# Optimization experiments

Measured on AMD Instinct MI355X. Metric: run time of the kernel, lower is better.

## Reference

```python
import jax, jax.numpy as jnp
import numpy as np

PROJ_DIM = 16384  # self.projDim / output_dim
THRESH = 1e-8     # self.thresh


def setup_inputs() -> dict:
    key = jax.random.key(0)
    k1, k2, k3, k4, k5 = jax.random.split(key, 5)
    B, C, H, W = 16, 2048, 14, 14
    x = jax.random.normal(k1, (B, C, H, W), dtype=jnp.float32)
    # count-sketch hash indices and Rademacher signs (fixed random params of CBP)
    h1 = jax.random.randint(k2, (C,), 0, PROJ_DIM, dtype=jnp.int32)
    h2 = jax.random.randint(k3, (C,), 0, PROJ_DIM, dtype=jnp.int32)
    w1 = (2 * jax.random.randint(k4, (C,), 0, 2) - 1).astype(jnp.float32)
    w2 = (2 * jax.random.randint(k5, (C,), 0, 2) - 1).astype(jnp.float32)
    return {"x": x, "w1": w1, "w2": w2, "h1": h1, "h2": h2}


def _count_sketch(xf, w, h):
    # xf: (N, C); scatter-add signed features into PROJ_DIM bins per location
    N = xf.shape[0]
    return jnp.zeros((N, PROJ_DIM), xf.dtype).at[:, h].add(xf * w)


def reference(x, w1, w2, h1, h2):
    B, C, H, W = x.shape
    # (B, C, H, W) -> (B*H*W, C): one feature vector per spatial location
    xf = x.transpose(0, 2, 3, 1).reshape(B * H * W, C)
    s1 = _count_sketch(xf, w1, h1)  # (N, D)
    s2 = _count_sketch(xf, w2, h2)  # (N, D)
    # circular convolution of the two sketches via FFT (real input -> rfft)
    y = jnp.fft.irfft(jnp.fft.rfft(s1, axis=-1) * jnp.fft.rfft(s2, axis=-1),
                      n=PROJ_DIM, axis=-1)  # (N, D)
    # sum-pool over spatial locations
    y = y.reshape(B, H * W, PROJ_DIM).sum(axis=1)  # (B, D)
    # signed sqrt + L2 normalization
    y = jnp.sign(y) * jnp.sqrt(jnp.abs(y) + THRESH)
    y = y / jnp.sqrt(jnp.sum(y * y, axis=-1, keepdims=True) + THRESH)
    return y  # (B, 16384), already flat as in torch.flatten(..., 1)
```

## Files before the change

### kernel.cpp

```cpp
#include <hip/hip_runtime.h>


#define D_PROJ 16384
#define C_CH   2048
#define HW_N   196
#define NKS    7
#define KPAD   (NKS * 32)
#define B_N    16
#define THREADS 512
#define NT     64
#define BUFS   6
#define ROWSH  448
#define TILE_SH (16 * ROWSH)
#define FPSCALE 65536.0f
#define INVSCALE (1.0f / 65536.0f)

typedef short  short8 __attribute__((ext_vector_type(8)));
typedef float  f32x4  __attribute__((ext_vector_type(4)));
typedef int    i32x4  __attribute__((ext_vector_type(4)));

static __device__ inline unsigned short f2bf(float f) {
    union { float f; unsigned u; } a; a.f = f;
    unsigned u = a.u;
    return (unsigned short)((u + 0x7FFFu + ((u >> 16) & 1u)) >> 16);
}
static __device__ inline float bf2f(unsigned short h) {
    union { unsigned u; float f; } a; a.u = ((unsigned)h) << 16;
    return a.f;
}
static __device__ inline f32x4 mfma16(short8 a, short8 b, f32x4 c) {
    return __builtin_amdgcn_mfma_f32_16x16x32_bf16(a, b, c, 0, 0, 0);
}

static __device__ inline void lds_iadd(int* p, int v) {
    unsigned off = (unsigned)(uintptr_t)p;
    asm volatile("ds_add_u32 %0, %1" :: "v"(off), "v"(v) : "memory");
}
static __device__ inline void lds_fadd(float* p, float v) {
    unsigned off = (unsigned)(uintptr_t)p;
    asm volatile("ds_add_f32 %0, %1" :: "v"(off), "v"(v) : "memory");
}
static __device__ inline void lds_drain() {
    asm volatile("s_waitcnt lgkmcnt(0)" ::: "memory");
    __builtin_amdgcn_sched_barrier(0);
}

static __device__ inline int swz_off(int ks, int lo64, int sub16, int row7) {
    return (((ks << 7) | lo64 | (sub16 << 4)) ^ (row7 << 4));
}

__global__ __launch_bounds__(256)
void cbp_convert(const float* __restrict__ x, unsigned short* __restrict__ ws) {
    const int id = blockIdx.x * 256 + threadIdx.x;
    const int total = B_N * C_CH * (KPAD / 8);
    if (id >= total) return;
    const int row = id / (KPAD / 8);
    const int sub = id - row * (KPAD / 8);
    const int k0  = sub * 8;
    const int ks  = k0 >> 5;
    const int s16 = (k0 >> 3) & 3;

    const float* xr = x + (size_t)row * HW_N;
    float v[8];
    if (k0 + 8 <= HW_N) {
        f32x4 p0 = *(const f32x4*)(xr + k0);
        f32x4 p1 = *(const f32x4*)(xr + k0 + 4);
#pragma unroll
        for (int e = 0; e < 4; ++e) { v[e] = p0[e]; v[4 + e] = p1[e]; }
    } else {
#pragma unroll
        for (int e = 0; e < 8; ++e) {
            const int k = k0 + e;
            v[e] = (k < HW_N) ? xr[k] : 0.0f;
        }
    }
    short8 hv, lv;
#pragma unroll
    for (int e = 0; e < 8; ++e) {
        unsigned short h = f2bf(v[e]);
        hv[e] = (short)h;
        lv[e] = (short)f2bf(v[e] - bf2f(h));
    }
    char* rowB = (char*)ws + (size_t)row * (ROWSH * 2);
    const int r7 = row & 7;
    *(short8*)(rowB + swz_off(ks, 0,  s16, r7)) = hv;
    *(short8*)(rowB + swz_off(ks, 64, s16, r7)) = lv;
}

static __device__ inline void stage_issue(const unsigned short* __restrict__ src0,
                                          unsigned short* dst0, int wave, int lane) {
    if (lane < 56) {
#pragma unroll
        for (int hlf = 0; hlf < 2; ++hlf) {
            const int row = wave + hlf * 8;
            const unsigned short* s = src0 + (size_t)row * ROWSH + (size_t)lane * 8;
            unsigned short* d = dst0 + (size_t)row * ROWSH;
            __builtin_amdgcn_global_load_lds(
                (const __attribute__((address_space(1))) void*)s,
                (__attribute__((address_space(3))) void*)d, 16, 0, 0);
        }
    }
}

__global__ __launch_bounds__(THREADS, 2)
void cbp_gram12(const unsigned short* __restrict__ ws,
                const float* __restrict__ w1f,
                const float* __restrict__ w2f,
                const int*   __restrict__ h1,
                const int*   __restrict__ h2,
                int*         __restrict__ part) {
    __shared__ __align__(16) int hist[D_PROJ];
    __shared__ __align__(16) unsigned short stage[BUFS][TILE_SH];
    __shared__ int pairsh[1024];

    const int id   = blockIdx.x;
    const int b    = ((id & 7) << 1) | ((id >> 3) & 1);
    const int rest = id >> 4;
    const int j0   = (rest & 1) * 1024;
    const int i0   = (rest >> 1) * 256;

    const int tid  = threadIdx.x;
    const int wave = tid >> 6;
    const int lane = tid & 63;
    const int l15  = lane & 15;
    const int lgrp = lane >> 4;
    const int r7s  = (l15 & 7) << 4;

    for (int t = tid; t < D_PROJ / 4; t += THREADS)
        ((i32x4*)hist)[t] = i32x4{0, 0, 0, 0};
    for (int t = tid; t < 1024; t += THREADS)
        pairsh[t] = h2[j0 + t] | (w2f[j0 + t] < 0.f ? (int)0x80000000 : 0);

    short8 ah[2][NKS], al[2][NKS];
    int    binr[2][4];
    float  s1s[2][4];
#pragma unroll
    for (int s = 0; s < 2; ++s) {
        const int irow = i0 + wave * 32 + s * 16 + l15;
        const char* rowA = (const char*)(ws + ((size_t)b * C_CH + irow) * ROWSH);
#pragma unroll
        for (int ks = 0; ks < NKS; ++ks) {
            ah[s][ks] = *(const short8*)(rowA + (((ks << 7) | (lgrp << 4)) ^ r7s));
            al[s][ks] = *(const short8*)(rowA + (((ks << 7) | 64 | (lgrp << 4)) ^ r7s));
        }
#pragma unroll
        for (int r = 0; r < 4; ++r) {
            const int ir = i0 + wave * 32 + s * 16 + lgrp * 4 + r;
            binr[s][r] = h1[ir];
            s1s[s][r]  = w1f[ir] * FPSCALE;
        }
    }

    const unsigned short* jbase = ws + ((size_t)b * C_CH + j0) * ROWSH;
#pragma unroll
    for (int p = 0; p < 4; ++p)
        stage_issue(jbase + (size_t)p * TILE_SH, stage[p], wave, lane);
    asm volatile("s_waitcnt lgkmcnt(0)" ::: "memory");

    for (int t = 0; t < NT; t += 2) {
        asm volatile("s_waitcnt vmcnt(4)" ::: "memory");
        __builtin_amdgcn_sched_barrier(0);
        asm volatile("s_barrier" ::: "memory");
        __builtin_amdgcn_sched_barrier(0);

        const int rb = t % BUFS;
#pragma unroll
        for (int half = 0; half < 2; ++half) {
            const int tt  = t + half;
            const char* srow = (const char*)&stage[rb + half][(size_t)l15 * ROWSH];
            f32x4 a0 = {0.f,0.f,0.f,0.f}, a1 = {0.f,0.f,0.f,0.f};
            f32x4 b0 = {0.f,0.f,0.f,0.f}, b1 = {0.f,0.f,0.f,0.f};
#pragma unroll
            for (int ks = 0; ks < NKS; ++ks) {
                const short8 bh = *(const short8*)(srow + (((ks << 7) | (lgrp << 4)) ^ r7s));
                const short8 bl = *(const short8*)(srow + (((ks << 7) | 64 | (lgrp << 4)) ^ r7s));
                if (ks & 1) {
                    a1 = mfma16(ah[0][ks], bh, a1);  b1 = mfma16(ah[1][ks], bh, b1);
                    a1 = mfma16(al[0][ks], bh, a1);  b1 = mfma16(al[1][ks], bh, b1);
                    a1 = mfma16(ah[0][ks], bl, a1);  b1 = mfma16(ah[1][ks], bl, b1);
                } else {
                    a0 = mfma16(ah[0][ks], bh, a0);  b0 = mfma16(ah[1][ks], bh, b0);
                    a0 = mfma16(al[0][ks], bh, a0);  b0 = mfma16(al[1][ks], bh, b0);
                    a0 = mfma16(ah[0][ks], bl, a0);  b0 = mfma16(ah[1][ks], bl, b0);
                }
            }
            const unsigned pk  = (unsigned)pairsh[tt * 16 + l15];
            const int      h2v = (int)(pk & 0x3FFFu);
            const unsigned sg2 = pk & 0x80000000u;
            const f32x4 g0 = a0 + a1;
            const f32x4 g1 = b0 + b1;
#pragma unroll
            for (int r = 0; r < 4; ++r) {
                int bin = binr[0][r] + h2v;
                if (bin >= D_PROJ) bin -= D_PROJ;
                const float fv = __uint_as_float(__float_as_uint(g0[r] * s1s[0][r]) ^ sg2);
                lds_iadd(&hist[bin], (int)rintf(fv));
            }
#pragma unroll
            for (int r = 0; r < 4; ++r) {
                int bin = binr[1][r] + h2v;
                if (bin >= D_PROJ) bin -= D_PROJ;
                const float fv = __uint_as_float(__float_as_uint(g1[r] * s1s[1][r]) ^ sg2);
                lds_iadd(&hist[bin], (int)rintf(fv));
            }
        }

        int t4 = t + 4; if (t4 > NT - 1) t4 = NT - 1;
        int t5 = t + 5; if (t5 > NT - 1) t5 = NT - 1;
        const int sb = (t + 4) % BUFS;
        stage_issue(jbase + (size_t)t4 * TILE_SH, stage[sb],     wave, lane);
        stage_issue(jbase + (size_t)t5 * TILE_SH, stage[sb + 1], wave, lane);
    }

    lds_drain();
    __syncthreads();
    int* pslot = part + (size_t)(b * 16 + rest) * D_PROJ;
    for (int t = tid; t < D_PROJ / 4; t += THREADS)
        ((i32x4*)pslot)[t] = ((const i32x4*)hist)[t];
}

__global__ void cbp_finalize2(const int* __restrict__ part, float* __restrict__ y) {
    const int b   = blockIdx.x;
    const int tid = threadIdx.x;
    const int* pb = part + (size_t)b * 16 * D_PROJ;
    float* yb = y + (size_t)b * D_PROJ;
    __shared__ float partial[4];

    float ssum = 0.f;
    for (int t = tid; t < D_PROJ; t += 256) {
        int acc = 0;
#pragma unroll
        for (int s = 0; s < 16; ++s) acc += pb[(size_t)s * D_PROJ + t];
        float v = (float)acc * INVSCALE;
        float sg = copysignf(sqrtf(fabsf(v) + 1e-8f), v);
        yb[t] = sg;
        ssum += sg * sg;
    }
    const int lane = tid & 63, wv = tid >> 6;
#pragma unroll
    for (int off = 32; off > 0; off >>= 1) ssum += __shfl_down(ssum, off, 64);
    if (lane == 0) partial[wv] = ssum;
    __syncthreads();
    const float total = partial[0] + partial[1] + partial[2] + partial[3];
    const float inv = 1.0f / sqrtf(total + 1e-8f);
    for (int t = tid; t < D_PROJ; t += 256) yb[t] *= inv;
}

static __device__ inline void cvt_split(const float (&v)[8], short8& hi, short8& lo) {
#pragma unroll
    for (int e = 0; e < 8; ++e) {
        unsigned short h = f2bf(v[e]);
        hi[e] = (short)h;
        lo[e] = (short)f2bf(v[e] - bf2f(h));
    }
}

__global__ __launch_bounds__(256, 2)
void cbp_gram_scatter(const float* __restrict__ x,
                      const float* __restrict__ w1f,
                      const float* __restrict__ w2f,
                      const int*   __restrict__ h1,
                      const int*   __restrict__ h2,
                      float*       __restrict__ y) {
    __shared__ float hist[D_PROJ];
    const int b    = blockIdx.y;
    const int i0   = blockIdx.x * 64;
    const int tid  = threadIdx.x;
    const int wave = tid >> 6;
    const int lane = tid & 63;
    const int l15  = lane & 15;
    const int lgrp = lane >> 4;

    for (int t = tid; t < D_PROJ; t += 256) hist[t] = 0.0f;
    const float* xb = x + (size_t)b * (C_CH * HW_N);

    const int    irow = i0 + wave * 16 + l15;
    const float* xa   = xb + (size_t)irow * HW_N;
    const float  w1s  = w1f[irow];
    short8 a_hi[NKS], a_lo[NKS];
#pragma unroll
    for (int ks = 0; ks < NKS; ++ks) {
        const int k0 = ks * 32 + lgrp * 8;
        float v[8];
#pragma unroll
        for (int e = 0; e < 8; ++e) {
            const int k = k0 + e;
            v[e] = (k < HW_N) ? xa[k] * w1s : 0.0f;
        }
        cvt_split(v, a_hi[ks], a_lo[ks]);
    }
    int bin1[4];
#pragma unroll
    for (int r = 0; r < 4; ++r) bin1[r] = h1[i0 + wave * 16 + lgrp * 4 + r];

    __syncthreads();

    for (int jt = 0; jt < C_CH / 16; ++jt) {
        const int    jrow = jt * 16 + l15;
        const float* xj   = xb + (size_t)jrow * HW_N;
        const float  w2s  = w2f[jrow];
        const int    h2j  = h2[jrow];
        f32x4 acc0 = {0.f, 0.f, 0.f, 0.f};
        f32x4 acc1 = {0.f, 0.f, 0.f, 0.f};
#pragma unroll
        for (int ks = 0; ks < NKS; ++ks) {
            const int k0 = ks * 32 + lgrp * 8;
            float v[8];
            if (ks < 6) {
                f32x4 p0 = *(const f32x4*)(xj + k0);
                f32x4 p1 = *(const f32x4*)(xj + k0 + 4);
#pragma unroll
                for (int e = 0; e < 4; ++e) { v[e] = p0[e]; v[4 + e] = p1[e]; }
            } else {
#pragma unroll
                for (int e = 0; e < 8; ++e) {
                    const int k = k0 + e;
                    v[e] = (k < HW_N) ? xj[k] : 0.0f;
                }
            }
#pragma unroll
            for (int e = 0; e < 8; ++e) v[e] *= w2s;
            short8 bhi, blo;
            cvt_split(v, bhi, blo);
            if (ks & 1) {
                acc1 = mfma16(a_hi[ks], bhi, acc1);
                acc1 = mfma16(a_hi[ks], blo, acc1);
                acc1 = mfma16(a_lo[ks], bhi, acc1);
            } else {
                acc0 = mfma16(a_hi[ks], bhi, acc0);
                acc0 = mfma16(a_hi[ks], blo, acc0);
                acc0 = mfma16(a_lo[ks], bhi, acc0);
            }
        }
        const f32x4 g = acc0 + acc1;
#pragma unroll
        for (int r = 0; r < 4; ++r) {
            int bin = bin1[r] + h2j;
            if (bin >= D_PROJ) bin -= D_PROJ;
            lds_fadd(&hist[bin], g[r]);
        }
    }

    lds_drain();
    __syncthreads();
    float* yb = y + (size_t)b * D_PROJ;
    for (int t = tid; t < D_PROJ; t += 256)
        atomicAdd(&yb[t], hist[t]);
}

__global__ void cbp_finalize(float* __restrict__ y) {
    const int b   = blockIdx.x;
    const int tid = threadIdx.x;
    float* yb = y + (size_t)b * D_PROJ;
    __shared__ float partial[4];

    float ssum = 0.f;
    for (int t = tid; t < D_PROJ; t += 256) {
        float v = yb[t];
        float s = copysignf(sqrtf(fabsf(v) + 1e-8f), v);
        yb[t] = s;
        ssum += s * s;
    }
    const int lane = tid & 63, wv = tid >> 6;
#pragma unroll
    for (int off = 32; off > 0; off >>= 1) ssum += __shfl_down(ssum, off, 64);
    if (lane == 0) partial[wv] = ssum;
    __syncthreads();
    const float total = partial[0] + partial[1] + partial[2] + partial[3];
    const float inv = 1.0f / sqrtf(total + 1e-8f);
    for (int t = tid; t < D_PROJ; t += 256) yb[t] *= inv;
}

extern "C" void kernel_launch(void* const* d_in, const int* in_sizes, int n_in,
                              void* d_out, int out_size, void* d_ws, size_t ws_size,
                              hipStream_t stream) {
    const float* x  = (const float*)d_in[0];
    const float* w1 = (const float*)d_in[1];
    const float* w2 = (const float*)d_in[2];
    const int*   h1 = (const int*)d_in[3];
    const int*   h2 = (const int*)d_in[4];
    float* y = (float*)d_out;

    const size_t need = (size_t)B_N * C_CH * ROWSH * 2 * sizeof(unsigned short);
    const size_t planeBytes = (size_t)B_N * C_CH * ROWSH * sizeof(unsigned short);

    if (ws_size >= need) {
        unsigned short* wsp = (unsigned short*)d_ws;
        int* part = (int*)((char*)d_ws + planeBytes);
        const int total = B_N * C_CH * (KPAD / 8);
        cbp_convert<<<(total + 255) / 256, 256, 0, stream>>>(x, wsp);
        cbp_gram12<<<256, THREADS, 0, stream>>>(wsp, w1, w2, h1, h2, part);
        cbp_finalize2<<<B_N, 256, 0, stream>>>(part, y);
    } else {
        hipMemsetAsync(y, 0, (size_t)B_N * D_PROJ * sizeof(float), stream);
        dim3 grid(C_CH / 64, B_N);
        cbp_gram_scatter<<<grid, 256, 0, stream>>>(x, w1, w2, h1, h2, y);
        cbp_finalize<<<B_N, 256, 0, stream>>>(y);
    }
}
```

Before: 132.5 us.

## Halve block threads and give each wave four register-held A row sets

The gram kernel moves from 8 waves holding 32 A rows each to 4 waves holding 64 rows each (SETS=4). Each LDS-staged B fragment is then reused across twice as many MFMAs, which cuts LDS read traffic per FLOP. Staging is rebalanced so each wave issues 4 row loads per tile, and the vmcnt wait is adjusted to match. The cost is much higher register pressure (launch bounds drop to 1 block per SIMD-set) and fewer waves to hide LDS-atomic and load latency.

Result: slower. 162.8 us (+22.9%).

```diff
diff --git a/kernel.cpp b/kernel.cpp
--- a/kernel.cpp
+++ b/kernel.cpp
@@ -7,7 +7,8 @@
 #define NKS    7
 #define KPAD   (NKS * 32)
 #define B_N    16
-#define THREADS 512
+#define THREADS 256
+#define SETS   4
 #define NT     64
 #define BUFS   6
 #define ROWSH  448
@@ -91,8 +92,8 @@
                                           unsigned short* dst0, int wave, int lane) {
     if (lane < 56) {
 #pragma unroll
-        for (int hlf = 0; hlf < 2; ++hlf) {
-            const int row = wave + hlf * 8;
+        for (int hlf = 0; hlf < 4; ++hlf) {
+            const int row = wave + hlf * 4;
             const unsigned short* s = src0 + (size_t)row * ROWSH + (size_t)lane * 8;
             unsigned short* d = dst0 + (size_t)row * ROWSH;
             __builtin_amdgcn_global_load_lds(
@@ -102,8 +103,8 @@
     }
 }
 
-__global__ __launch_bounds__(THREADS, 2)
-void cbp_gram12(const unsigned short* __restrict__ ws,
+__global__ __launch_bounds__(THREADS, 1)
+void cbp_gram13(const unsigned short* __restrict__ ws,
                 const float* __restrict__ w1f,
                 const float* __restrict__ w2f,
                 const int*   __restrict__ h1,
@@ -131,12 +132,12 @@
     for (int t = tid; t < 1024; t += THREADS)
         pairsh[t] = h2[j0 + t] | (w2f[j0 + t] < 0.f ? (int)0x80000000 : 0);
 
-    short8 ah[2][NKS], al[2][NKS];
-    int    binr[2][4];
-    float  s1s[2][4];
-#pragma unroll
-    for (int s = 0; s < 2; ++s) {
-        const int irow = i0 + wave * 32 + s * 16 + l15;
+    short8 ah[SETS][NKS], al[SETS][NKS];
+    int    binr[SETS][4];
+    float  s1s[SETS][4];
+#pragma unroll
+    for (int s = 0; s < SETS; ++s) {
+        const int irow = i0 + wave * 64 + s * 16 + l15;
         const char* rowA = (const char*)(ws + ((size_t)b * C_CH + irow) * ROWSH);
 #pragma unroll
         for (int ks = 0; ks < NKS; ++ks) {
@@ -145,7 +146,7 @@
         }
 #pragma unroll
         for (int r = 0; r < 4; ++r) {
-            const int ir = i0 + wave * 32 + s * 16 + lgrp * 4 + r;
+            const int ir = i0 + wave * 64 + s * 16 + lgrp * 4 + r;
             binr[s][r] = h1[ir];
             s1s[s][r]  = w1f[ir] * FPSCALE;
         }
@@ -158,7 +159,7 @@
     asm volatile("s_waitcnt lgkmcnt(0)" ::: "memory");
 
     for (int t = 0; t < NT; t += 2) {
-        asm volatile("s_waitcnt vmcnt(4)" ::: "memory");
+        asm volatile("s_waitcnt vmcnt(8)" ::: "memory");
         __builtin_amdgcn_sched_barrier(0);
         asm volatile("s_barrier" ::: "memory");
         __builtin_amdgcn_sched_barrier(0);
@@ -168,40 +169,45 @@
         for (int half = 0; half < 2; ++half) {
             const int tt  = t + half;
             const char* srow = (const char*)&stage[rb + half][(size_t)l15 * ROWSH];
-            f32x4 a0 = {0.f,0.f,0.f,0.f}, a1 = {0.f,0.f,0.f,0.f};
-            f32x4 b0 = {0.f,0.f,0.f,0.f}, b1 = {0.f,0.f,0.f,0.f};
+            f32x4 acc0[SETS], acc1[SETS];
+#pragma unroll
+            for (int s = 0; s < SETS; ++s) {
+                acc0[s] = f32x4{0.f, 0.f, 0.f, 0.f};
+                acc1[s] = f32x4{0.f, 0.f, 0.f, 0.f};
+            }
 #pragma unroll
             for (int ks = 0; ks < NKS; ++ks) {
                 const short8 bh = *(const short8*)(srow + (((ks << 7) | (lgrp << 4)) ^ r7s));
                 const short8 bl = *(const short8*)(srow + (((ks << 7) | 64 | (lgrp << 4)) ^ r7s));
                 if (ks & 1) {
-                    a1 = mfma16(ah[0][ks], bh, a1);  b1 = mfma16(ah[1][ks], bh, b1);
-                    a1 = mfma16(al[0][ks], bh, a1);  b1 = mfma16(al[1][ks], bh, b1);
-                    a1 = mfma16(ah[0][ks], bl, a1);  b1 = mfma16(ah[1][ks], bl, b1);
+#pragma unroll
+                    for (int s = 0; s < SETS; ++s) {
+                        acc1[s] = mfma16(ah[s][ks], bh, acc1[s]);
+                        acc1[s] = mfma16(al[s][ks], bh, acc1[s]);
+                        acc1[s] = mfma16(ah[s][ks], bl, acc1[s]);
+                    }
                 } else {
-                    a0 = mfma16(ah[0][ks], bh, a0);  b0 = mfma16(ah[1][ks], bh, b0);
-                    a0 = mfma16(al[0][ks], bh, a0);  b0 = mfma16(al[1][ks], bh, b0);
-                    a0 = mfma16(ah[0][ks], bl, a0);  b0 = mfma16(ah[1][ks], bl, b0);
+#pragma unroll
+                    for (int s = 0; s < SETS; ++s) {
+                        acc0[s] = mfma16(ah[s][ks], bh, acc0[s]);
+                        acc0[s] = mfma16(al[s][ks], bh, acc0[s]);
+                        acc0[s] = mfma16(ah[s][ks], bl, acc0[s]);
+                    }
                 }
             }
             const unsigned pk  = (unsigned)pairsh[tt * 16 + l15];
             const int      h2v = (int)(pk & 0x3FFFu);
             const unsigned sg2 = pk & 0x80000000u;
-            const f32x4 g0 = a0 + a1;
-            const f32x4 g1 = b0 + b1;
-#pragma unroll
-            for (int r = 0; r < 4; ++r) {
-                int bin = binr[0][r] + h2v;
-                if (bin >= D_PROJ) bin -= D_PROJ;
-                const float fv = __uint_as_float(__float_as_uint(g0[r] * s1s[0][r]) ^ sg2);
-                lds_iadd(&hist[bin], (int)rintf(fv));
-            }
-#pragma unroll
-            for (int r = 0; r < 4; ++r) {
-                int bin = binr[1][r] + h2v;
-                if (bin >= D_PROJ) bin -= D_PROJ;
-                const float fv = __uint_as_float(__float_as_uint(g1[r] * s1s[1][r]) ^ sg2);
-                lds_iadd(&hist[bin], (int)rintf(fv));
+#pragma unroll
+            for (int s = 0; s < SETS; ++s) {
+                const f32x4 g = acc0[s] + acc1[s];
+#pragma unroll
+                for (int r = 0; r < 4; ++r) {
+                    int bin = binr[s][r] + h2v;
+                    if (bin >= D_PROJ) bin -= D_PROJ;
+                    const float fv = __uint_as_float(__float_as_uint(g[r] * s1s[s][r]) ^ sg2);
+                    lds_iadd(&hist[bin], (int)rintf(fv));
+                }
             }
         }
 
@@ -389,7 +395,7 @@
         int* part = (int*)((char*)d_ws + planeBytes);
         const int total = B_N * C_CH * (KPAD / 8);
         cbp_convert<<<(total + 255) / 256, 256, 0, stream>>>(x, wsp);
-        cbp_gram12<<<256, THREADS, 0, stream>>>(wsp, w1, w2, h1, h2, part);
+        cbp_gram13<<<256, THREADS, 0, stream>>>(wsp, w1, w2, h1, h2, part);
         cbp_finalize2<<<B_N, 256, 0, stream>>>(part, y);
     } else {
         hipMemsetAsync(y, 0, (size_t)B_N * D_PROJ * sizeof(float), stream);
```
